# Kernel optimization log

Hardware: AMD Instinct MI355X
Metric: run time of the kernel (lower is better)

Reference implementation:

```python
import jax, jax.numpy as jnp
import numpy as np

MUL = 64          # multiplicity of every irrep block
N = 200000        # batch (e.g. edges in an equivariant GNN)
SQRT3 = 3.0 ** 0.5

# Levi-Civita tensor: real-basis Wigner 3j for 1x1->1 is eps/sqrt(6);
# e3nn's (y,z,x) ordering is a cyclic permutation so eps is unchanged.
_eps = np.zeros((3, 3, 3), dtype=np.float32)
for (i, j, k), s in {(0,1,2): 1, (1,2,0): 1, (2,0,1): 1,
                     (0,2,1): -1, (2,1,0): -1, (1,0,2): -1}.items():
    _eps[i, j, k] = s
EPS = jnp.asarray(_eps)


def setup_inputs() -> dict:
    key = jax.random.key(0)
    ks = jax.random.split(key, 7)
    return {
        "x1": jax.random.normal(ks[0], (N, 4 * MUL), jnp.float32),   # 64x0e + 64x1o
        "x2": jax.random.normal(ks[1], (N, 4), jnp.float32),          # 1x0e + 1x1o
        "w_ss_s": jax.random.normal(ks[2], (MUL, 1, MUL), jnp.float32),  # ins (0,0,0)
        "w_vv_s": jax.random.normal(ks[3], (MUL, 1, MUL), jnp.float32),  # ins (1,1,0)
        "w_sv_v": jax.random.normal(ks[4], (MUL, 1, MUL), jnp.float32),  # ins (0,1,1)
        "w_vs_v": jax.random.normal(ks[5], (MUL, 1, MUL), jnp.float32),  # ins (1,0,1)
        "w_vv_v": jax.random.normal(ks[6], (MUL, 1, MUL), jnp.float32),  # ins (1,1,1)
    }


def reference(x1, x2, w_ss_s, w_vv_s, w_sv_v, w_vs_v, w_vv_v):
    n = x1.shape[0]
    # split irreps blocks
    x1s = x1[:, :MUL]                        # [z,u]      64x0e
    x1v = x1[:, MUL:].reshape(n, MUL, 3)     # [z,u,i]    64x1o
    x2s = x2[:, :1]                          # [z,v]      1x0e
    x2v = x2[:, 1:].reshape(n, 1, 3)         # [z,v,j]    1x1o

    # e3nn path normalization (component norm, all vars/path_weights = 1):
    # alpha = sqrt(1 / sum_{ins -> same i_out} mul1*mul2)
    a0 = (1.0 / (2 * MUL)) ** 0.5            # scalar out: fan-in 64 + 64
    a1 = (1.0 / (3 * MUL)) ** 0.5            # vector out: fan-in 64 * 3

    # Wigner 3j (real basis) * sqrt(2*l_out+1)  [component normalization]:
    #   0x0->0 : 1        0x1->1, 1x0->1 : delta
    #   1x1->0 : delta/sqrt(3)     1x1->1 : eps/sqrt(2)
    out_s = a0 * (jnp.einsum('uvw,zu,zv->zw', w_ss_s, x1s, x2s)
                  + (1.0 / SQRT3) * jnp.einsum('uvw,zui,zvi->zw', w_vv_s, x1v, x2v))

    out_v = a1 * (jnp.einsum('uvw,zu,zvk->zwk', w_sv_v, x1s, x2v)
                  + jnp.einsum('uvw,zuk,zv->zwk', w_vs_v, x1v, x2s)
                  + (2.0 ** -0.5) * jnp.einsum('uvw,ijk,zui,zvj->zwk', w_vv_v, EPS, x1v, x2v))

    return jnp.concatenate([out_s, out_v.reshape(n, 3 * MUL)], axis=1)
```

## Files before the change

kernel.cpp:

```cpp
#include <hip/hip_runtime.h>

#define BLOCK 512
#define RPG   32

__global__ __launch_bounds__(BLOCK, 4) void tp_kernel(
    const float* __restrict__ x1, const float* __restrict__ x2,
    const float* __restrict__ w0, const float* __restrict__ w1,
    const float* __restrict__ w2, const float* __restrict__ w3,
    const float* __restrict__ w4,
    float* __restrict__ out, int n)
{
    __shared__ __align__(16) float lds_w[5 * 4096];

    const int t = threadIdx.x;

    {
        const float* srcs[5] = {w0, w1, w2, w3, w4};
        #pragma unroll
        for (int m = 0; m < 5; ++m) {
            const float4* s = (const float4*)srcs[m];
            float4* d = (float4*)(&lds_w[m * 4096]);
            for (int i = t; i < 1024; i += BLOCK) d[i] = s[i];
        }
    }
    __syncthreads();

    const int g = t & 15;
    const int r = t >> 4;

    const float a0  = 0.088388347648318447f;
    const float a1  = 0.072168783648703216f;
    const float is3 = 0.57735026918962576f;
    const float is2 = 0.70710678118654752f;

    const int ngroups = (n + RPG - 1) / RPG;
    for (int grp = blockIdx.x; grp < ngroups; grp += (int)gridDim.x) {
        const int z   = grp * RPG + r;
        const bool act = (z < n);
        const float* xrow = x1 + (size_t)(act ? z : 0) * 256;

        float yss[4], ysv[4], yvvs[4][3], yvs[4][3], yvvv[4][3];
        #pragma unroll
        for (int j = 0; j < 4; ++j) {
            yss[j] = 0.f; ysv[j] = 0.f;
            #pragma unroll
            for (int i = 0; i < 3; ++i) { yvvs[j][i] = 0.f; yvs[j][i] = 0.f; yvvv[j][i] = 0.f; }
        }

        #pragma unroll 1
        for (int uc = 0; uc < 8; ++uc) {
            alignas(16) float sarr[8];
            alignas(16) float varr[24];
            *(float4*)(sarr + 0) = *(const float4*)(xrow + uc * 8 + 0);
            *(float4*)(sarr + 4) = *(const float4*)(xrow + uc * 8 + 4);
            #pragma unroll
            for (int k = 0; k < 6; ++k)
                *(float4*)(varr + 4 * k) = *(const float4*)(xrow + 64 + uc * 24 + 4 * k);

            #pragma unroll
            for (int q = 0; q < 8; ++q) {
                const int u = uc * 8 + q;
                const float4 wss  = *(const float4*)(&lds_w[0 * 4096 + u * 64 + 4 * g]);
                const float4 wvvs = *(const float4*)(&lds_w[1 * 4096 + u * 64 + 4 * g]);
                const float4 wsv  = *(const float4*)(&lds_w[2 * 4096 + u * 64 + 4 * g]);
                const float4 wvs  = *(const float4*)(&lds_w[3 * 4096 + u * 64 + 4 * g]);
                const float4 wvvv = *(const float4*)(&lds_w[4 * 4096 + u * 64 + 4 * g]);

                const float s  = sarr[q];
                const float vx = varr[3 * q + 0];
                const float vy = varr[3 * q + 1];
                const float vz = varr[3 * q + 2];

                const float* wssf  = (const float*)&wss;
                const float* wvvsf = (const float*)&wvvs;
                const float* wsvf  = (const float*)&wsv;
                const float* wvsf  = (const float*)&wvs;
                const float* wvvvf = (const float*)&wvvv;

                #pragma unroll
                for (int j = 0; j < 4; ++j) {
                    yss[j]     += wssf[j]  * s;
                    ysv[j]     += wsvf[j]  * s;
                    yvvs[j][0] += wvvsf[j] * vx;
                    yvvs[j][1] += wvvsf[j] * vy;
                    yvvs[j][2] += wvvsf[j] * vz;
                    yvs[j][0]  += wvsf[j]  * vx;
                    yvs[j][1]  += wvsf[j]  * vy;
                    yvs[j][2]  += wvsf[j]  * vz;
                    yvvv[j][0] += wvvvf[j] * vx;
                    yvvv[j][1] += wvvvf[j] * vy;
                    yvvv[j][2] += wvvvf[j] * vz;
                }
            }
        }

        if (act) {
            const float4 x2v = *(const float4*)(x2 + (size_t)z * 4);
            const float s2  = x2v.x;
            const float v2x = x2v.y;
            const float v2y = x2v.z;
            const float v2z = x2v.w;
            float* orow = out + (size_t)z * 256;
            alignas(16) float os[4];
            alignas(16) float ov[12];
            #pragma unroll
            for (int j = 0; j < 4; ++j) {
                os[j] = a0 * (yss[j] * s2
                      + is3 * (yvvs[j][0] * v2x + yvvs[j][1] * v2y + yvvs[j][2] * v2z));
                const float cx = yvvv[j][1] * v2z - yvvv[j][2] * v2y;
                const float cy = yvvv[j][2] * v2x - yvvv[j][0] * v2z;
                const float cz = yvvv[j][0] * v2y - yvvv[j][1] * v2x;
                ov[3*j+0] = a1 * (ysv[j] * v2x + yvs[j][0] * s2 + is2 * cx);
                ov[3*j+1] = a1 * (ysv[j] * v2y + yvs[j][1] * s2 + is2 * cy);
                ov[3*j+2] = a1 * (ysv[j] * v2z + yvs[j][2] * s2 + is2 * cz);
            }
            *(float4*)(orow + 4*g)           = *(float4*)os;
            *(float4*)(orow + 64 + 12*g + 0) = *(float4*)(ov + 0);
            *(float4*)(orow + 64 + 12*g + 4) = *(float4*)(ov + 4);
            *(float4*)(orow + 64 + 12*g + 8) = *(float4*)(ov + 8);
        }
    }
}

extern "C" void kernel_launch(void* const* d_in, const int* in_sizes, int n_in,
                              void* d_out, int out_size, void* d_ws, size_t ws_size,
                              hipStream_t stream) {
    const float* x1 = (const float*)d_in[0];
    const float* x2 = (const float*)d_in[1];
    const float* w0 = (const float*)d_in[2];
    const float* w1 = (const float*)d_in[3];
    const float* w2 = (const float*)d_in[4];
    const float* w3 = (const float*)d_in[5];
    const float* w4 = (const float*)d_in[6];
    float* out = (float*)d_out;
    const int n = in_sizes[0] / 256;
    tp_kernel<<<512, BLOCK, 0, stream>>>(x1, x2, w0, w1, w2, w3, w4, out, n);
}
```

Before: 622.3 us.

## Remap threads so lanes own rows and waves own output columns

```diff
diff --git a/kernel.cpp b/kernel.cpp
--- a/kernel.cpp
+++ b/kernel.cpp
@@ -1,124 +1,134 @@
 #include <hip/hip_runtime.h>
 
 #define BLOCK 512
-#define RPG   32
+#define RPG   64
 
-__global__ __launch_bounds__(BLOCK, 4) void tp_kernel(
+#define DO_U(u_, s_, vx_, vy_, vz_) { \
+    const float4 wss  = *(const float4*)(&lds_w[0*2048 + (u_)*32 + lc]); \
+    const float4 wvvs = *(const float4*)(&lds_w[1*2048 + (u_)*32 + lc]); \
+    const float4 wsv  = *(const float4*)(&lds_w[2*2048 + (u_)*32 + lc]); \
+    const float4 wvs  = *(const float4*)(&lds_w[3*2048 + (u_)*32 + lc]); \
+    const float4 wvvv = *(const float4*)(&lds_w[4*2048 + (u_)*32 + lc]); \
+    const float* wssf  = (const float*)&wss;  \
+    const float* wvvsf = (const float*)&wvvs; \
+    const float* wsvf  = (const float*)&wsv;  \
+    const float* wvsf  = (const float*)&wvs;  \
+    const float* wvvvf = (const float*)&wvvv; \
+    _Pragma("unroll") \
+    for (int j = 0; j < 4; ++j) { \
+        yss[j]     += wssf[j]  * (s_);  \
+        ysv[j]     += wsvf[j]  * (s_);  \
+        yvvs[j][0] += wvvsf[j] * (vx_); \
+        yvvs[j][1] += wvvsf[j] * (vy_); \
+        yvvs[j][2] += wvvsf[j] * (vz_); \
+        yvs[j][0]  += wvsf[j]  * (vx_); \
+        yvs[j][1]  += wvsf[j]  * (vy_); \
+        yvs[j][2]  += wvsf[j]  * (vz_); \
+        yvvv[j][0] += wvvvf[j] * (vx_); \
+        yvvv[j][1] += wvvvf[j] * (vy_); \
+        yvvv[j][2] += wvvvf[j] * (vz_); \
+    } \
+}
+
+#define DO_CHUNK(UB, S, V0, V1, V2) \
+    DO_U((UB)+0, (S).x, (V0).x, (V0).y, (V0).z) \
+    DO_U((UB)+1, (S).y, (V0).w, (V1).x, (V1).y) \
+    DO_U((UB)+2, (S).z, (V1).z, (V1).w, (V2).x) \
+    DO_U((UB)+3, (S).w, (V2).y, (V2).z, (V2).w)
+
+__global__ __launch_bounds__(BLOCK) void tp_kernel(
     const float* __restrict__ x1, const float* __restrict__ x2,
     const float* __restrict__ w0, const float* __restrict__ w1,
     const float* __restrict__ w2, const float* __restrict__ w3,
     const float* __restrict__ w4,
     float* __restrict__ out, int n)
 {
-    __shared__ __align__(16) float lds_w[5 * 4096];
+    __shared__ __align__(16) float lds_w[5 * 2048];
 
-    const int t = threadIdx.x;
+    const int t    = threadIdx.x;
+    const int half = blockIdx.x & 1;
+    const int grp  = blockIdx.x >> 1;
+    const int wv   = t >> 6;
+    const int lane = t & 63;
+    const int lc   = 4 * wv;
 
     {
         const float* srcs[5] = {w0, w1, w2, w3, w4};
         #pragma unroll
         for (int m = 0; m < 5; ++m) {
-            const float4* s = (const float4*)srcs[m];
-            float4* d = (float4*)(&lds_w[m * 4096]);
-            for (int i = t; i < 1024; i += BLOCK) d[i] = s[i];
+            for (int i = t; i < 512; i += BLOCK) {
+                const int u  = i >> 3;
+                const int c4 = i & 7;
+                *(float4*)(&lds_w[m * 2048 + u * 32 + 4 * c4]) =
+                    *(const float4*)(srcs[m] + u * 64 + half * 32 + 4 * c4);
+            }
         }
     }
     __syncthreads();
 
-    const int g = t & 15;
-    const int r = t >> 4;
+    const int z    = grp * RPG + lane;
+    const bool act = (z < n);
+    const float* xrow = x1 + (size_t)(act ? z : 0) * 256;
 
-    const float a0  = 0.088388347648318447f;
-    const float a1  = 0.072168783648703216f;
-    const float is3 = 0.57735026918962576f;
-    const float is2 = 0.70710678118654752f;
+    float yss[4], ysv[4], yvvs[4][3], yvs[4][3], yvvv[4][3];
+    #pragma unroll
+    for (int j = 0; j < 4; ++j) {
+        yss[j] = 0.f; ysv[j] = 0.f;
+        #pragma unroll
+        for (int i = 0; i < 3; ++i) { yvvs[j][i] = 0.f; yvs[j][i] = 0.f; yvvv[j][i] = 0.f; }
+    }
 
-    const int ngroups = (n + RPG - 1) / RPG;
-    for (int grp = blockIdx.x; grp < ngroups; grp += (int)gridDim.x) {
-        const int z   = grp * RPG + r;
-        const bool act = (z < n);
-        const float* xrow = x1 + (size_t)(act ? z : 0) * 256;
+    float4 sA  = *(const float4*)(xrow + 0);
+    float4 vA0 = *(const float4*)(xrow + 64 + 0);
+    float4 vA1 = *(const float4*)(xrow + 64 + 4);
+    float4 vA2 = *(const float4*)(xrow + 64 + 8);
+    float4 sB, vB0, vB1, vB2;
 
-        float yss[4], ysv[4], yvvs[4][3], yvs[4][3], yvvv[4][3];
+    #pragma unroll 1
+    for (int c = 0; c < 16; c += 2) {
+        sB  = *(const float4*)(xrow + 4 * (c + 1));
+        vB0 = *(const float4*)(xrow + 64 + 12 * (c + 1) + 0);
+        vB1 = *(const float4*)(xrow + 64 + 12 * (c + 1) + 4);
+        vB2 = *(const float4*)(xrow + 64 + 12 * (c + 1) + 8);
+        DO_CHUNK(4 * c, sA, vA0, vA1, vA2);
+        if (c + 2 < 16) {
+            sA  = *(const float4*)(xrow + 4 * (c + 2));
+            vA0 = *(const float4*)(xrow + 64 + 12 * (c + 2) + 0);
+            vA1 = *(const float4*)(xrow + 64 + 12 * (c + 2) + 4);
+            vA2 = *(const float4*)(xrow + 64 + 12 * (c + 2) + 8);
+        }
+        DO_CHUNK(4 * c + 4, sB, vB0, vB1, vB2);
+    }
+
+    if (act) {
+        const float a0  = 0.088388347648318447f;
+        const float a1  = 0.072168783648703216f;
+        const float is3 = 0.57735026918962576f;
+        const float is2 = 0.70710678118654752f;
+        const float4 x2v = *(const float4*)(x2 + (size_t)z * 4);
+        const float s2  = x2v.x;
+        const float v2x = x2v.y;
+        const float v2y = x2v.z;
+        const float v2z = x2v.w;
+        float* orow = out + (size_t)z * 256;
+        const int gc = half * 32 + lc;
+        alignas(16) float os[4];
+        alignas(16) float ov[12];
         #pragma unroll
         for (int j = 0; j < 4; ++j) {
-            yss[j] = 0.f; ysv[j] = 0.f;
-            #pragma unroll
-            for (int i = 0; i < 3; ++i) { yvvs[j][i] = 0.f; yvs[j][i] = 0.f; yvvv[j][i] = 0.f; }
+            os[j] = a0 * (yss[j] * s2
+                  + is3 * (yvvs[j][0] * v2x + yvvs[j][1] * v2y + yvvs[j][2] * v2z));
+            const float cx = yvvv[j][1] * v2z - yvvv[j][2] * v2y;
+            const float cy = yvvv[j][2] * v2x - yvvv[j][0] * v2z;
+            const float cz = yvvv[j][0] * v2y - yvvv[j][1] * v2x;
+            ov[3*j+0] = a1 * (ysv[j] * v2x + yvs[j][0] * s2 + is2 * cx);
+            ov[3*j+1] = a1 * (ysv[j] * v2y + yvs[j][1] * s2 + is2 * cy);
+            ov[3*j+2] = a1 * (ysv[j] * v2z + yvs[j][2] * s2 + is2 * cz);
         }
-
-        #pragma unroll 1
-        for (int uc = 0; uc < 8; ++uc) {
-            alignas(16) float sarr[8];
-            alignas(16) float varr[24];
-            *(float4*)(sarr + 0) = *(const float4*)(xrow + uc * 8 + 0);
-            *(float4*)(sarr + 4) = *(const float4*)(xrow + uc * 8 + 4);
-            #pragma unroll
-            for (int k = 0; k < 6; ++k)
-                *(float4*)(varr + 4 * k) = *(const float4*)(xrow + 64 + uc * 24 + 4 * k);
-
-            #pragma unroll
-            for (int q = 0; q < 8; ++q) {
-                const int u = uc * 8 + q;
-                const float4 wss  = *(const float4*)(&lds_w[0 * 4096 + u * 64 + 4 * g]);
-                const float4 wvvs = *(const float4*)(&lds_w[1 * 4096 + u * 64 + 4 * g]);
-                const float4 wsv  = *(const float4*)(&lds_w[2 * 4096 + u * 64 + 4 * g]);
-                const float4 wvs  = *(const float4*)(&lds_w[3 * 4096 + u * 64 + 4 * g]);
-                const float4 wvvv = *(const float4*)(&lds_w[4 * 4096 + u * 64 + 4 * g]);
-
-                const float s  = sarr[q];
-                const float vx = varr[3 * q + 0];
-                const float vy = varr[3 * q + 1];
-                const float vz = varr[3 * q + 2];
-
-                const float* wssf  = (const float*)&wss;
-                const float* wvvsf = (const float*)&wvvs;
-                const float* wsvf  = (const float*)&wsv;
-                const float* wvsf  = (const float*)&wvs;
-                const float* wvvvf = (const float*)&wvvv;
-
-                #pragma unroll
-                for (int j = 0; j < 4; ++j) {
-                    yss[j]     += wssf[j]  * s;
-                    ysv[j]     += wsvf[j]  * s;
-                    yvvs[j][0] += wvvsf[j] * vx;
-                    yvvs[j][1] += wvvsf[j] * vy;
-                    yvvs[j][2] += wvvsf[j] * vz;
-                    yvs[j][0]  += wvsf[j]  * vx;
-                    yvs[j][1]  += wvsf[j]  * vy;
-                    yvs[j][2]  += wvsf[j]  * vz;
-                    yvvv[j][0] += wvvvf[j] * vx;
-                    yvvv[j][1] += wvvvf[j] * vy;
-                    yvvv[j][2] += wvvvf[j] * vz;
-                }
-            }
-        }
-
-        if (act) {
-            const float4 x2v = *(const float4*)(x2 + (size_t)z * 4);
-            const float s2  = x2v.x;
-            const float v2x = x2v.y;
-            const float v2y = x2v.z;
-            const float v2z = x2v.w;
-            float* orow = out + (size_t)z * 256;
-            alignas(16) float os[4];
-            alignas(16) float ov[12];
-            #pragma unroll
-            for (int j = 0; j < 4; ++j) {
-                os[j] = a0 * (yss[j] * s2
-                      + is3 * (yvvs[j][0] * v2x + yvvs[j][1] * v2y + yvvs[j][2] * v2z));
-                const float cx = yvvv[j][1] * v2z - yvvv[j][2] * v2y;
-                const float cy = yvvv[j][2] * v2x - yvvv[j][0] * v2z;
-                const float cz = yvvv[j][0] * v2y - yvvv[j][1] * v2x;
-                ov[3*j+0] = a1 * (ysv[j] * v2x + yvs[j][0] * s2 + is2 * cx);
-                ov[3*j+1] = a1 * (ysv[j] * v2y + yvs[j][1] * s2 + is2 * cy);
-                ov[3*j+2] = a1 * (ysv[j] * v2z + yvs[j][2] * s2 + is2 * cz);
-            }
-            *(float4*)(orow + 4*g)           = *(float4*)os;
-            *(float4*)(orow + 64 + 12*g + 0) = *(float4*)(ov + 0);
-            *(float4*)(orow + 64 + 12*g + 4) = *(float4*)(ov + 4);
-            *(float4*)(orow + 64 + 12*g + 8) = *(float4*)(ov + 8);
-        }
+        *(float4*)(orow + gc)              = *(float4*)os;
+        *(float4*)(orow + 64 + 3*gc + 0)   = *(float4*)(ov + 0);
+        *(float4*)(orow + 64 + 3*gc + 4)   = *(float4*)(ov + 4);
+        *(float4*)(orow + 64 + 3*gc + 8)   = *(float4*)(ov + 8);
     }
 }
 
@@ -134,5 +144,6 @@
     const float* w4 = (const float*)d_in[6];
     float* out = (float*)d_out;
     const int n = in_sizes[0] / 256;
-    tp_kernel<<<512, BLOCK, 0, stream>>>(x1, x2, w0, w1, w2, w3, w4, out, n);
+    const int ngroups = (n + RPG - 1) / RPG;
+    tp_kernel<<<2 * ngroups, BLOCK, 0, stream>>>(x1, x2, w0, w1, w2, w3, w4, out, n);
 }
```

After: 771.8 us. 1.24x slower.
